# Kernel tuning notes

Measured on AMD Instinct MI355X. Metric: run time of the kernel, lower is better.

Reference implementation:

```python
import jax, jax.numpy as jnp
import numpy as np

LOG_2PI = float(np.log(2.0 * np.pi))


def setup_inputs() -> dict:
    key = jax.random.key(0)
    k1, k2, k3 = jax.random.split(key, 3)
    N, D, K = 2_000_000, 16, 32
    data = jax.random.normal(k1, (N, D), dtype=jnp.float32)
    means = jax.random.uniform(k2, (K, D), dtype=jnp.float32)  # torch.rand init
    # torch init is eye expanded per component; perturb slightly so the
    # Cholesky / solve paths are exercised with non-trivial values while
    # A @ A.T stays well-conditioned PD.
    cov_parts = (jnp.eye(D, dtype=jnp.float32)[None, :, :]
                 + 0.1 * jax.random.normal(k3, (K, D, D), dtype=jnp.float32))
    log_weights = jnp.zeros((K,), dtype=jnp.float32)
    return {"data": data, "means": means, "cov_parts": cov_parts,
            "log_weights": log_weights}


def _mixture_loglik(data, means, cov_parts, log_weights):
    D = data.shape[-1]
    # covariance_k = A_k @ A_k^T  -> Cholesky factor L_k (lower)
    cov = jnp.einsum('kij,klj->kil', cov_parts, cov_parts)      # [K, D, D]
    chol = jnp.linalg.cholesky(cov)                             # [K, D, D]

    def comp_logprob(mu, L):
        # MVN log_prob for one component over all N points
        diff = data - mu                                        # [N, D]
        # solve L z = diff^T  -> z: [D, N]
        z = jax.scipy.linalg.solve_triangular(L, diff.T, lower=True)
        quad = jnp.sum(z * z, axis=0)                           # [N]
        logdet = jnp.sum(jnp.log(jnp.diagonal(L)))              # 0.5*logdet(cov)
        return -0.5 * (quad + D * LOG_2PI) - logdet             # [N]

    # [N, K] log-likelihood per point per component
    log_liks = jax.vmap(comp_logprob, in_axes=(0, 0), out_axes=1)(means, chol)
    weighted = log_liks + log_weights ** 2                      # note: squared, per source
    return jnp.mean(jax.nn.logsumexp(weighted, axis=1))


def reference(data, means, cov_parts, log_weights):
    return _mixture_loglik(data, means, cov_parts, log_weights)
```

## Files before the change

kernel.cpp:

```cpp
#include <hip/hip_runtime.h>
#include <math.h>


#define LOG_2PI 1.8378770664093453f
#define INV_LN2 1.4426950408889634f
#define LN2_D   0.6931471805599453

typedef float    float4v __attribute__((ext_vector_type(4)));
typedef float    f32x16  __attribute__((ext_vector_type(16)));
typedef _Float16 f16x8   __attribute__((ext_vector_type(8)));
typedef _Float16 f16x2   __attribute__((ext_vector_type(2)));

union H8 { f16x8 h8; f16x2 h2[4]; };

#if __has_builtin(__builtin_amdgcn_exp2f)
#define EXP2F(x) __builtin_amdgcn_exp2f(x)
#else
#define EXP2F(x) exp2f(x)
#endif
#if __has_builtin(__builtin_amdgcn_logf)
#define LOG2F(x) __builtin_amdgcn_logf(x)
#else
#define LOG2F(x) log2f(x)
#endif

static __device__ __forceinline__ f16x2 pk2(float a, float b) {
#if __has_builtin(__builtin_amdgcn_cvt_pkrtz)
  return __builtin_bit_cast(f16x2, __builtin_amdgcn_cvt_pkrtz(a, b));
#else
  f16x2 r; r[0] = (_Float16)a; r[1] = (_Float16)b; return r;
#endif
}

static __device__ __forceinline__ float partner32(float x, bool lo) {
#if __has_builtin(__builtin_amdgcn_permlane32_swap)
  typedef unsigned u32x2 __attribute__((ext_vector_type(2)));
  unsigned u = __builtin_bit_cast(unsigned, x);
  u32x2 r = __builtin_amdgcn_permlane32_swap(u, u, false, false);
  return __builtin_bit_cast(float, lo ? r[1] : r[0]);
#else
  return __shfl_xor(x, 32, 64);
#endif
}

static __device__ __forceinline__ f16x2 sel2(bool c, f16x2 a, f16x2 b) {
  unsigned ua = __builtin_bit_cast(unsigned, a);
  unsigned ub = __builtin_bit_cast(unsigned, b);
  return __builtin_bit_cast(f16x2, c ? ua : ub);
}

__global__ void setup_kernel(const float* __restrict__ means,
                             const float* __restrict__ cov_parts,
                             const float* __restrict__ log_weights,
                             _Float16* __restrict__ W)
{
  const int k = blockIdx.x;
  const int i = threadIdx.x;

  __shared__ float sA[16][17];
  __shared__ float sC[16][17];
  __shared__ float sMu[16];
  __shared__ float sR[16];

  if (i < 16) {
    #pragma unroll
    for (int j = 0; j < 16; ++j) sA[i][j] = cov_parts[(k*16 + i)*16 + j];
    sMu[i] = means[k*16 + i];
  }
  __syncthreads();

  if (i < 16) {
    #pragma unroll
    for (int j = 0; j < 16; ++j) {
      float acc = 0.f;
      #pragma unroll
      for (int l = 0; l < 16; ++l) acc += sA[i][l] * sA[j][l];
      sC[i][j] = acc;
    }
  }
  __syncthreads();

  for (int j = 0; j < 16; ++j) {
    if (i == j) {
      float d = sC[j][j];
      for (int l = 0; l < j; ++l) d -= sC[j][l]*sC[j][l];
      sC[j][j] = sqrtf(d);
    }
    __syncthreads();
    if (i < 16 && i > j) {
      float a = sC[i][j];
      for (int l = 0; l < j; ++l) a -= sC[i][l]*sC[j][l];
      sC[i][j] = a / sC[j][j];
    }
    __syncthreads();
  }

  if (i < 16) {
    float y[16];
    #pragma unroll
    for (int r = 0; r < 16; ++r) {
      float a = (r == i) ? 1.f : 0.f;
      #pragma unroll
      for (int l = 0; l < r; ++l) a -= sC[r][l] * y[l];
      y[r] = a / sC[r][r];
    }
    #pragma unroll
    for (int r = 0; r < 16; ++r) sA[r][i] = y[r];
  }
  __syncthreads();

  if (i < 16) {
    float p[16];
    #pragma unroll
    for (int j = 0; j < 16; ++j) {
      float acc = 0.f;
      #pragma unroll
      for (int l = 0; l < 16; ++l) acc += sA[l][i] * sA[l][j];
      p[j] = acc;
    }
    float ri = 0.f;
    #pragma unroll
    for (int j = 0; j < 16; ++j) ri += p[j] * sMu[j];
    sR[i] = ri;

    #pragma unroll
    for (int j = 0; j < 16; ++j) {
      W[(size_t)(i*64 + (k + 32*(j >> 3)))*8 + (j & 7)] =
          (_Float16)(-0.5f * INV_LN2 * p[j]);
    }
    W[(size_t)(16*64 + (k + 32*(i >> 3)))*8 + (i & 7)] =
        (_Float16)(INV_LN2 * ri);
  }
  __syncthreads();

  if (i == 0) {
    float logdet = 0.f;
    #pragma unroll
    for (int j = 0; j < 16; ++j) logdet += __logf(sC[j][j]);
    float mupmu = 0.f;
    #pragma unroll
    for (int j = 0; j < 16; ++j) mupmu += sMu[j] * sR[j];
    float lw = log_weights[k];
    float c2v = INV_LN2 * (-0.5f*(mupmu + 16.f*LOG_2PI) - logdet + lw*lw);
    #pragma unroll
    for (int v = 0; v < 8; ++v) {
      W[(size_t)(17*64 + k)*8 + v]      = (v == 0) ? (_Float16)c2v : (_Float16)0.f;
      W[(size_t)(17*64 + k + 32)*8 + v] = (_Float16)0.f;
    }
  }
}

__global__ __launch_bounds__(256, 2) void main_kernel(
    const float* __restrict__ data,
    const _Float16* __restrict__ W,
    float* __restrict__ partials,
    int npairs)
{
  const int lane = threadIdx.x & 63;
  const int n32  = lane & 31;
  const bool lo  = lane < 32;
  const int gwave  = (int)((blockIdx.x * blockDim.x + threadIdx.x) >> 6);
  const int nwaves = (int)((gridDim.x * blockDim.x) >> 6);

  f16x8 Wf[18];
  #pragma unroll
  for (int c = 0; c < 18; ++c)
    Wf[c] = *(const f16x8*)(W + (size_t)(c*64 + lane)*8);

  H8 bC;
  #pragma unroll
  for (int j = 0; j < 4; ++j) bC.h2[j] = pk2(0.f, 0.f);
  if (lo) bC.h2[0] = pk2(1.f, 0.f);

  float accsum = 0.f;

  const char* ptr = (const char*)data + ((size_t)gwave*4096 + (size_t)n32*64);
  const size_t step = (size_t)nwaves * 4096;

  float4v pA0, pA1, pA2, pA3, pB0, pB1, pB2, pB3;
  if (gwave < npairs) {
    pA0 = *(const float4v*)(ptr);        pA1 = *(const float4v*)(ptr + 16);
    pA2 = *(const float4v*)(ptr + 32);   pA3 = *(const float4v*)(ptr + 48);
    pB0 = *(const float4v*)(ptr + 2048); pB1 = *(const float4v*)(ptr + 2064);
    pB2 = *(const float4v*)(ptr + 2080); pB3 = *(const float4v*)(ptr + 2096);
  }

  for (int p = gwave; p < npairs; p += nwaves) {
    f16x2 xhA[8], xhB[8];
    xhA[0] = pk2(pA0[0], pA0[1]); xhA[1] = pk2(pA0[2], pA0[3]);
    xhA[2] = pk2(pA1[0], pA1[1]); xhA[3] = pk2(pA1[2], pA1[3]);
    xhA[4] = pk2(pA2[0], pA2[1]); xhA[5] = pk2(pA2[2], pA2[3]);
    xhA[6] = pk2(pA3[0], pA3[1]); xhA[7] = pk2(pA3[2], pA3[3]);
    xhB[0] = pk2(pB0[0], pB0[1]); xhB[1] = pk2(pB0[2], pB0[3]);
    xhB[2] = pk2(pB1[0], pB1[1]); xhB[3] = pk2(pB1[2], pB1[3]);
    xhB[4] = pk2(pB2[0], pB2[1]); xhB[5] = pk2(pB2[2], pB2[3]);
    xhB[6] = pk2(pB3[0], pB3[1]); xhB[7] = pk2(pB3[2], pB3[3]);

    ptr += step;
    if (p + nwaves < npairs) {
      pA0 = *(const float4v*)(ptr);        pA1 = *(const float4v*)(ptr + 16);
      pA2 = *(const float4v*)(ptr + 32);   pA3 = *(const float4v*)(ptr + 48);
      pB0 = *(const float4v*)(ptr + 2048); pB1 = *(const float4v*)(ptr + 2064);
      pB2 = *(const float4v*)(ptr + 2080); pB3 = *(const float4v*)(ptr + 2096);
    }

    f16x2 xsA[4], xsB[4];
    #pragma unroll
    for (int j = 0; j < 4; ++j) {
      xsA[j] = sel2(lo, xhA[j], xhA[4+j]);
      xsB[j] = sel2(lo, xhB[j], xhB[4+j]);
    }

    f32x16 accA, accB;
    #pragma unroll
    for (int r = 0; r < 16; ++r) { accA[r] = 0.f; accB[r] = 0.f; }

    #pragma unroll
    for (int c = 0; c < 16; ++c) {
      _Float16 xiA = xhA[c >> 1][c & 1];
      H8 bA;
      #pragma unroll
      for (int j = 0; j < 4; ++j) bA.h2[j] = xsA[j] * xiA;
      accA = __builtin_amdgcn_mfma_f32_32x32x16_f16(Wf[c], bA.h8, accA, 0, 0, 0);
      _Float16 xiB = xhB[c >> 1][c & 1];
      H8 bB;
      #pragma unroll
      for (int j = 0; j < 4; ++j) bB.h2[j] = xsB[j] * xiB;
      accB = __builtin_amdgcn_mfma_f32_32x32x16_f16(Wf[c], bB.h8, accB, 0, 0, 0);
    }
    {
      H8 bA, bB;
      #pragma unroll
      for (int j = 0; j < 4; ++j) { bA.h2[j] = xsA[j]; bB.h2[j] = xsB[j]; }
      accA = __builtin_amdgcn_mfma_f32_32x32x16_f16(Wf[16], bA.h8, accA, 0, 0, 0);
      accB = __builtin_amdgcn_mfma_f32_32x32x16_f16(Wf[16], bB.h8, accB, 0, 0, 0);
    }
    {
      accA = __builtin_amdgcn_mfma_f32_32x32x16_f16(Wf[17], bC.h8, accA, 0, 0, 0);
      accB = __builtin_amdgcn_mfma_f32_32x32x16_f16(Wf[17], bC.h8, accB, 0, 0, 0);
    }

    {
      float m = accA[0];
      #pragma unroll
      for (int r = 1; r < 16; ++r) m = fmaxf(m, accA[r]);
      m = fmaxf(m, partner32(m, lo));
      float s = 0.f;
      #pragma unroll
      for (int r = 0; r < 16; ++r) s += EXP2F(accA[r] - m);
      s += partner32(s, lo);
      accsum += m + LOG2F(s);
    }
    {
      float m = accB[0];
      #pragma unroll
      for (int r = 1; r < 16; ++r) m = fmaxf(m, accB[r]);
      m = fmaxf(m, partner32(m, lo));
      float s = 0.f;
      #pragma unroll
      for (int r = 0; r < 16; ++r) s += EXP2F(accB[r] - m);
      s += partner32(s, lo);
      accsum += m + LOG2F(s);
    }
  }

  #pragma unroll
  for (int off = 1; off <= 32; off <<= 1)
    accsum += __shfl_xor(accsum, off, 64);

  __shared__ float wsum[4];
  const int wid = (int)(threadIdx.x >> 6);
  if ((threadIdx.x & 63) == 0) wsum[wid] = accsum;
  __syncthreads();
  if (threadIdx.x == 0)
    partials[blockIdx.x] = wsum[0] + wsum[1] + wsum[2] + wsum[3];
}

__global__ void reduce_kernel(const float* __restrict__ partials, int n,
                              float* __restrict__ out, double scale)
{
  __shared__ double sd[256];
  double a = 0.0;
  for (int idx = threadIdx.x; idx < n; idx += 256) a += (double)partials[idx];
  sd[threadIdx.x] = a;
  __syncthreads();
  for (int s = 128; s > 0; s >>= 1) {
    if ((int)threadIdx.x < s) sd[threadIdx.x] += sd[threadIdx.x + s];
    __syncthreads();
  }
  if (threadIdx.x == 0) out[0] = (float)(sd[0] * scale);
}

extern "C" void kernel_launch(void* const* d_in, const int* in_sizes, int n_in,
                              void* d_out, int out_size, void* d_ws, size_t ws_size,
                              hipStream_t stream)
{
  const float* data        = (const float*)d_in[0];
  const float* means       = (const float*)d_in[1];
  const float* cov_parts   = (const float*)d_in[2];
  const float* log_weights = (const float*)d_in[3];

  const int npts   = in_sizes[0] / 16;
  const int npairs = npts / 64;

  _Float16* W      = (_Float16*)d_ws;
  float*    partials = (float*)((char*)d_ws + (size_t)18*64*8*sizeof(_Float16));

  const int GRID = 512, BLOCK = 256;
  setup_kernel<<<32, 64, 0, stream>>>(means, cov_parts, log_weights, W);
  main_kernel<<<GRID, BLOCK, 0, stream>>>(data, W, partials, npairs);
  reduce_kernel<<<1, 256, 0, stream>>>(partials, GRID, (float*)d_out,
                                       LN2_D / (2.0 * (double)npts));
}
```

Measured before the change: 202.9 us.

## Halve per-lane loads via half-row split with permlane swap, double-buffer prefetch

Each lane now loads only its half (32 bytes) of a point's 16 floats instead of the full row that was duplicated across the two wave halves. It then rebuilds the full row with a permlane32 swap. Prefetch depth goes from one to two iterations using two register slots, to hide more memory latency. This cuts redundant load instructions and cache traffic, at the cost of extra cross-lane swaps and selects, a clamped dummy load at the tail, and more register use.

```diff
diff --git a/kernel.cpp b/kernel.cpp
--- a/kernel.cpp
+++ b/kernel.cpp
@@ -32,17 +32,21 @@
 #endif
 }
 
-static __device__ __forceinline__ float partner32(float x, bool lo) {
+static __device__ __forceinline__ unsigned swapd(unsigned u, bool lo) {
 #if __has_builtin(__builtin_amdgcn_permlane32_swap)
   typedef unsigned u32x2 __attribute__((ext_vector_type(2)));
-  unsigned u = __builtin_bit_cast(unsigned, x);
   u32x2 r = __builtin_amdgcn_permlane32_swap(u, u, false, false);
-  return __builtin_bit_cast(float, lo ? r[1] : r[0]);
+  return lo ? r[1] : r[0];
 #else
-  return __shfl_xor(x, 32, 64);
+  return (unsigned)__shfl_xor((int)u, 32, 64);
 #endif
 }
-
+static __device__ __forceinline__ float partner32(float x, bool lo) {
+  return __builtin_bit_cast(float, swapd(__builtin_bit_cast(unsigned, x), lo));
+}
+static __device__ __forceinline__ f16x2 swap2(f16x2 v, bool lo) {
+  return __builtin_bit_cast(f16x2, swapd(__builtin_bit_cast(unsigned, v), lo));
+}
 static __device__ __forceinline__ f16x2 sel2(bool c, f16x2 a, f16x2 b) {
   unsigned ua = __builtin_bit_cast(unsigned, a);
   unsigned ub = __builtin_bit_cast(unsigned, b);
@@ -174,93 +178,107 @@
 
   float accsum = 0.f;
 
-  const char* ptr = (const char*)data + ((size_t)gwave*4096 + (size_t)n32*64);
-  const size_t step = (size_t)nwaves * 4096;
-
-  float4v pA0, pA1, pA2, pA3, pB0, pB1, pB2, pB3;
-  if (gwave < npairs) {
-    pA0 = *(const float4v*)(ptr);        pA1 = *(const float4v*)(ptr + 16);
-    pA2 = *(const float4v*)(ptr + 32);   pA3 = *(const float4v*)(ptr + 48);
-    pB0 = *(const float4v*)(ptr + 2048); pB1 = *(const float4v*)(ptr + 2064);
-    pB2 = *(const float4v*)(ptr + 2080); pB3 = *(const float4v*)(ptr + 2096);
-  }
-
-  for (int p = gwave; p < npairs; p += nwaves) {
-    f16x2 xhA[8], xhB[8];
-    xhA[0] = pk2(pA0[0], pA0[1]); xhA[1] = pk2(pA0[2], pA0[3]);
-    xhA[2] = pk2(pA1[0], pA1[1]); xhA[3] = pk2(pA1[2], pA1[3]);
-    xhA[4] = pk2(pA2[0], pA2[1]); xhA[5] = pk2(pA2[2], pA2[3]);
-    xhA[6] = pk2(pA3[0], pA3[1]); xhA[7] = pk2(pA3[2], pA3[3]);
-    xhB[0] = pk2(pB0[0], pB0[1]); xhB[1] = pk2(pB0[2], pB0[3]);
-    xhB[2] = pk2(pB1[0], pB1[1]); xhB[3] = pk2(pB1[2], pB1[3]);
-    xhB[4] = pk2(pB2[0], pB2[1]); xhB[5] = pk2(pB2[2], pB2[3]);
-    xhB[6] = pk2(pB3[0], pB3[1]); xhB[7] = pk2(pB3[2], pB3[3]);
-
-    ptr += step;
-    if (p + nwaves < npairs) {
-      pA0 = *(const float4v*)(ptr);        pA1 = *(const float4v*)(ptr + 16);
-      pA2 = *(const float4v*)(ptr + 32);   pA3 = *(const float4v*)(ptr + 48);
-      pB0 = *(const float4v*)(ptr + 2048); pB1 = *(const float4v*)(ptr + 2064);
-      pB2 = *(const float4v*)(ptr + 2080); pB3 = *(const float4v*)(ptr + 2096);
-    }
-
-    f16x2 xsA[4], xsB[4];
-    #pragma unroll
-    for (int j = 0; j < 4; ++j) {
-      xsA[j] = sel2(lo, xhA[j], xhA[4+j]);
-      xsB[j] = sel2(lo, xhB[j], xhB[4+j]);
-    }
-
-    f32x16 accA, accB;
-    #pragma unroll
-    for (int r = 0; r < 16; ++r) { accA[r] = 0.f; accB[r] = 0.f; }
-
-    #pragma unroll
-    for (int c = 0; c < 16; ++c) {
-      _Float16 xiA = xhA[c >> 1][c & 1];
-      H8 bA;
-      #pragma unroll
-      for (int j = 0; j < 4; ++j) bA.h2[j] = xsA[j] * xiA;
-      accA = __builtin_amdgcn_mfma_f32_32x32x16_f16(Wf[c], bA.h8, accA, 0, 0, 0);
-      _Float16 xiB = xhB[c >> 1][c & 1];
-      H8 bB;
-      #pragma unroll
-      for (int j = 0; j < 4; ++j) bB.h2[j] = xsB[j] * xiB;
-      accB = __builtin_amdgcn_mfma_f32_32x32x16_f16(Wf[c], bB.h8, accB, 0, 0, 0);
-    }
-    {
-      H8 bA, bB;
-      #pragma unroll
-      for (int j = 0; j < 4; ++j) { bA.h2[j] = xsA[j]; bB.h2[j] = xsB[j]; }
-      accA = __builtin_amdgcn_mfma_f32_32x32x16_f16(Wf[16], bA.h8, accA, 0, 0, 0);
-      accB = __builtin_amdgcn_mfma_f32_32x32x16_f16(Wf[16], bB.h8, accB, 0, 0, 0);
-    }
-    {
-      accA = __builtin_amdgcn_mfma_f32_32x32x16_f16(Wf[17], bC.h8, accA, 0, 0, 0);
-      accB = __builtin_amdgcn_mfma_f32_32x32x16_f16(Wf[17], bC.h8, accB, 0, 0, 0);
-    }
-
-    {
-      float m = accA[0];
-      #pragma unroll
-      for (int r = 1; r < 16; ++r) m = fmaxf(m, accA[r]);
-      m = fmaxf(m, partner32(m, lo));
-      float s = 0.f;
-      #pragma unroll
-      for (int r = 0; r < 16; ++r) s += EXP2F(accA[r] - m);
-      s += partner32(s, lo);
-      accsum += m + LOG2F(s);
-    }
-    {
-      float m = accB[0];
-      #pragma unroll
-      for (int r = 1; r < 16; ++r) m = fmaxf(m, accB[r]);
-      m = fmaxf(m, partner32(m, lo));
-      float s = 0.f;
-      #pragma unroll
-      for (int r = 0; r < 16; ++r) s += EXP2F(accB[r] - m);
-      s += partner32(s, lo);
-      accsum += m + LOG2F(s);
+  const char* base = (const char*)data + ((size_t)n32*64 + (lo ? 0 : 32));
+  auto paddr = [&](int p) { return base + (size_t)p*4096; };
+
+  float4v sa0[2], sa1[2], sb0[2], sb1[2];
+
+  {
+    const char* q0 = (gwave           < npairs) ? paddr(gwave)          : base;
+    const char* q1 = (gwave + nwaves  < npairs) ? paddr(gwave + nwaves) : base;
+    sa0[0] = *(const float4v*)(q0);        sa1[0] = *(const float4v*)(q0 + 16);
+    sb0[0] = *(const float4v*)(q0 + 2048); sb1[0] = *(const float4v*)(q0 + 2064);
+    sa0[1] = *(const float4v*)(q1);        sa1[1] = *(const float4v*)(q1 + 16);
+    sb0[1] = *(const float4v*)(q1 + 2048); sb1[1] = *(const float4v*)(q1 + 2064);
+  }
+
+  int p = gwave;
+  while (p < npairs) {
+    #pragma unroll
+    for (int slot = 0; slot < 2; ++slot) {
+      if (p >= npairs) break;
+
+      f16x2 ownA[4], ownB[4];
+      ownA[0] = pk2(sa0[slot][0], sa0[slot][1]);
+      ownA[1] = pk2(sa0[slot][2], sa0[slot][3]);
+      ownA[2] = pk2(sa1[slot][0], sa1[slot][1]);
+      ownA[3] = pk2(sa1[slot][2], sa1[slot][3]);
+      ownB[0] = pk2(sb0[slot][0], sb0[slot][1]);
+      ownB[1] = pk2(sb0[slot][2], sb0[slot][3]);
+      ownB[2] = pk2(sb1[slot][0], sb1[slot][1]);
+      ownB[3] = pk2(sb1[slot][2], sb1[slot][3]);
+
+      {
+        int np_ = p + 2*nwaves;
+        const char* q = (np_ < npairs) ? paddr(np_) : base;
+        sa0[slot] = *(const float4v*)(q);        sa1[slot] = *(const float4v*)(q + 16);
+        sb0[slot] = *(const float4v*)(q + 2048); sb1[slot] = *(const float4v*)(q + 2064);
+      }
+
+      f16x2 xhA[8], xhB[8];
+      #pragma unroll
+      for (int j = 0; j < 4; ++j) {
+        f16x2 oA = swap2(ownA[j], lo);
+        f16x2 oB = swap2(ownB[j], lo);
+        xhA[j]   = sel2(lo, ownA[j], oA);
+        xhA[4+j] = sel2(lo, oA, ownA[j]);
+        xhB[j]   = sel2(lo, ownB[j], oB);
+        xhB[4+j] = sel2(lo, oB, ownB[j]);
+      }
+
+      f32x16 accA, accB;
+      #pragma unroll
+      for (int r = 0; r < 16; ++r) { accA[r] = 0.f; accB[r] = 0.f; }
+
+      #pragma unroll
+      for (int c = 0; c < 16; ++c) {
+        _Float16 xiA = xhA[c >> 1][c & 1];
+        H8 bA;
+        #pragma unroll
+        for (int j = 0; j < 4; ++j) bA.h2[j] = ownA[j] * xiA;
+        accA = __builtin_amdgcn_mfma_f32_32x32x16_f16(Wf[c], bA.h8, accA, 0, 0, 0);
+        _Float16 xiB = xhB[c >> 1][c & 1];
+        H8 bB;
+        #pragma unroll
+        for (int j = 0; j < 4; ++j) bB.h2[j] = ownB[j] * xiB;
+        accB = __builtin_amdgcn_mfma_f32_32x32x16_f16(Wf[c], bB.h8, accB, 0, 0, 0);
+      }
+      {
+        H8 bA, bB;
+        #pragma unroll
+        for (int j = 0; j < 4; ++j) { bA.h2[j] = ownA[j]; bB.h2[j] = ownB[j]; }
+        accA = __builtin_amdgcn_mfma_f32_32x32x16_f16(Wf[16], bA.h8, accA, 0, 0, 0);
+        accB = __builtin_amdgcn_mfma_f32_32x32x16_f16(Wf[16], bB.h8, accB, 0, 0, 0);
+      }
+      {
+        accA = __builtin_amdgcn_mfma_f32_32x32x16_f16(Wf[17], bC.h8, accA, 0, 0, 0);
+        accB = __builtin_amdgcn_mfma_f32_32x32x16_f16(Wf[17], bC.h8, accB, 0, 0, 0);
+      }
+
+      {
+        float m = accA[0];
+        #pragma unroll
+        for (int r = 1; r < 16; ++r) m = fmaxf(m, accA[r]);
+        m = fmaxf(m, partner32(m, lo));
+        float s = 0.f;
+        #pragma unroll
+        for (int r = 0; r < 16; ++r) s += EXP2F(accA[r] - m);
+        s += partner32(s, lo);
+        accsum += m + LOG2F(s);
+      }
+      {
+        float m = accB[0];
+        #pragma unroll
+        for (int r = 1; r < 16; ++r) m = fmaxf(m, accB[r]);
+        m = fmaxf(m, partner32(m, lo));
+        float s = 0.f;
+        #pragma unroll
+        for (int r = 0; r < 16; ++r) s += EXP2F(accB[r] - m);
+        s += partner32(s, lo);
+        accsum += m + LOG2F(s);
+      }
+
+      p += nwaves;
     }
   }
 
```

After: 205.5 us. About the same (+1.3%).
